# Performance work log

Measured on AMD Instinct MI355X. Metric: run time of the kernel, lower is better.

The kernel has to match this reference:

```python
import jax, jax.numpy as jnp
import numpy as np

N_P, N_I, DIM = 30, 40, 6
W_I, C1, C2, LAM = 0.7, 1.5, 1.5, 0.3
EPS = 1e-8


def _decode(pos):
    # pos: [P, 6] -> per-particle fusion weights via pairwise softmax
    e = jnp.exp(pos[:, :4])
    fg_s = e[:, 0] + e[:, 1] + EPS
    bg_s = e[:, 2] + e[:, 3] + EPS
    return e[:, 0] / fg_s, e[:, 1] / fg_s, e[:, 2] / bg_s, e[:, 3] / bg_s


def _fitness(pos, rgb, dep, mask, r_dep):
    # rgb, dep, mask, r_dep: [H, W]; pos: [P, 6] -> scores [P]
    rgb_fg, dep_fg, rgb_bg, dep_bg = _decode(pos)
    mn = mask - mask.mean()
    mn_norm = jnp.linalg.norm(mn) + EPS
    fg = rgb_fg[:, None, None] * rgb + dep_fg[:, None, None] * dep   # [P,H,W]
    bg = rgb_bg[:, None, None] * rgb + dep_bg[:, None, None] * dep
    fused = mask * fg + (1.0 - mask) * bg
    fn = fused - fused.mean(axis=(1, 2), keepdims=True)
    fn_norm = jnp.sqrt((fn * fn).sum(axis=(1, 2)))
    ncc = (fn * mn).sum(axis=(1, 2)) / (fn_norm * mn_norm + EPS)
    pen_fg = ((1.0 - r_dep) * mask).mean()
    pen_bg = ((1.0 - r_dep) * (1.0 - mask)).mean()
    rel_pen = dep_fg * pen_fg + dep_bg * pen_bg
    return ncc - LAM * rel_pen


def _pso(rgb, dep, mask, r_dep):
    # Deterministic PSO with fixed RNG key; inputs are [H, W] maps.
    key = jax.random.key(42)
    k_pos, k_vel, k_r1, k_r2 = jax.random.split(key, 4)
    pos = jax.random.uniform(k_pos, (N_P, DIM), minval=-2.0, maxval=2.0)
    vel = jax.random.uniform(k_vel, (N_P, DIM), minval=-0.5, maxval=0.5)
    r1s = jax.random.uniform(k_r1, (N_I, N_P, DIM))
    r2s = jax.random.uniform(k_r2, (N_I, N_P, DIM))

    pb_pos = pos
    pb_fit = _fitness(pos, rgb, dep, mask, r_dep)
    gi = jnp.argmax(pb_fit)
    gb_pos = pb_pos[gi]
    gb_fit = pb_fit[gi]

    def step(carry, rs):
        pos, vel, pb_pos, pb_fit, gb_pos, gb_fit = carry
        r1, r2 = rs
        vel = W_I * vel + C1 * r1 * (pb_pos - pos) + C2 * r2 * (gb_pos - pos)
        pos = jnp.clip(pos + vel, -3.0, 3.0)
        fit = _fitness(pos, rgb, dep, mask, r_dep)
        better = fit > pb_fit
        pb_pos = jnp.where(better[:, None], pos, pb_pos)
        pb_fit = jnp.where(better, fit, pb_fit)
        bi = jnp.argmax(pb_fit)
        improve = pb_fit[bi] > gb_fit
        gb_pos = jnp.where(improve, pb_pos[bi], gb_pos)
        gb_fit = jnp.where(improve, pb_fit[bi], gb_fit)
        return (pos, vel, pb_pos, pb_fit, gb_pos, gb_fit), None

    (pos, vel, pb_pos, pb_fit, gb_pos, gb_fit), _ = jax.lax.scan(
        step, (pos, vel, pb_pos, pb_fit, gb_pos, gb_fit), (r1s, r2s))
    rgb_fg, dep_fg, rgb_bg, dep_bg = _decode(gb_pos[None, :])
    return rgb_fg[0], dep_fg[0], rgb_bg[0], dep_bg[0]


def _cos_sim(feat, proto):
    # feat [B,C,H,W], proto [B,C] -> [B,H,W]; matches F.normalize (clamp_min eps)
    p = proto / jnp.maximum(jnp.linalg.norm(proto, axis=1, keepdims=True), 1e-12)
    fnorm = jnp.maximum(jnp.sqrt((feat * feat).sum(axis=1, keepdims=True)), 1e-12)
    f = feat / fnorm
    return jnp.einsum('bchw,bc->bhw', f, p)


def setup_inputs() -> dict:
    key = jax.random.key(0)
    ks = jax.random.split(key, 10)
    B, C, H, W = 8, 256, 64, 64
    return {
        'f_rgb': jax.random.normal(ks[0], (B, C, H, W), dtype=jnp.float32),
        'f_depth': jax.random.normal(ks[1], (B, C, H, W), dtype=jnp.float32),
        'r_rgb': jax.random.uniform(ks[2], (B, 1, H, W), dtype=jnp.float32),
        'r_depth': jax.random.uniform(ks[3], (B, 1, H, W), dtype=jnp.float32),
        'proto_rgb': jax.random.normal(ks[4], (B, C), dtype=jnp.float32),
        'proto_dep': jax.random.normal(ks[5], (B, C), dtype=jnp.float32),
        'query_mask': jax.random.uniform(ks[6], (B, 1, H, W), dtype=jnp.float32),
        'conv_w': jax.random.normal(ks[7], (C, C), dtype=jnp.float32) * 0.05,
        'bn_gamma': jax.random.uniform(ks[8], (C,), dtype=jnp.float32),
        'bn_beta': jax.random.normal(ks[9], (C,), dtype=jnp.float32) * 0.1,
        'bn_mean': jnp.zeros((C,), dtype=jnp.float32),
        'bn_var': jnp.ones((C,), dtype=jnp.float32),
    }


def reference(f_rgb, f_depth, r_rgb, r_depth, proto_rgb, proto_dep, query_mask,
              conv_w, bn_gamma, bn_beta, bn_mean, bn_var):
    # cosine similarity maps [B,H,W]
    rgb_sim = _cos_sim(f_rgb, proto_rgb)
    dep_sim = _cos_sim(f_depth, proto_dep)

    # PSO operates on detached batch-mean maps (torch .detach().mean(0).cpu())
    sg = jax.lax.stop_gradient
    np_rgb = sg(rgb_sim).mean(axis=0)                 # [H,W]
    np_dep = sg(dep_sim).mean(axis=0)                 # [H,W]
    np_mask = sg(query_mask)[:, 0].mean(axis=0)       # mask already at (H,W): nearest interp is identity
    np_r_dep = sg(r_depth)[:, 0].mean(axis=0)
    rgb_fg, dep_fg, rgb_bg, dep_bg = _pso(np_rgb, np_dep, np_mask, np_r_dep)

    f_fg = rgb_fg * f_rgb + dep_fg * f_depth
    f_bg = rgb_bg * f_rgb + dep_bg * f_depth
    proxy = jax.nn.sigmoid((rgb_sim + dep_sim)[:, None] * 3.0)   # [B,1,H,W]
    f_fused = proxy * f_fg + (1.0 - proxy) * f_bg

    # post_proj: 1x1 conv (no bias) -> BN (eval) -> ReLU
    y = jnp.einsum('oc,bchw->bohw', conv_w, f_fused)
    inv = bn_gamma / jnp.sqrt(bn_var + 1e-5)
    y = y * inv[None, :, None, None] + (bn_beta - bn_mean * inv)[None, :, None, None]
    return jax.nn.relu(y)
```

## Files before the change

kernel.cpp:

```cpp
#include <hip/hip_runtime.h>
#include <stdint.h>
#include <float.h>

static constexpr size_t WS_SIM_RGB = 4096;
static constexpr size_t WS_SIM_DEP = 36864;
static constexpr size_t WS_NPMAPS  = 69632;
static constexpr size_t WS_SYNC    = 86048;
static constexpr size_t WS_RNG     = 90112;

typedef short short8 __attribute__((ext_vector_type(8)));
typedef float f32x4 __attribute__((ext_vector_type(4)));

static constexpr uint32_t SYNC_MAGIC = 0x5A17C0DEu;

__device__ __forceinline__ uint32_t pack_bf2(float a, float b) {
  uint32_t ua = __float_as_uint(a), ub = __float_as_uint(b);
  uint32_t ra = (ua + 0x7fffu + ((ua >> 16) & 1u)) >> 16;
  uint32_t rb = (ub + 0x7fffu + ((ub >> 16) & 1u)) >> 16;
  return (ra & 0xffffu) | (rb << 16);
}

__device__ __forceinline__ void threefry2x32(uint32_t k0, uint32_t k1,
                                             uint32_t c0, uint32_t c1,
                                             uint32_t& o0, uint32_t& o1) {
  uint32_t ks2 = k0 ^ k1 ^ 0x1BD11BDAu;
  uint32_t x0 = c0 + k0;
  uint32_t x1 = c1 + k1;
#define TF_ROUND(r) { x0 += x1; x1 = (x1 << (r)) | (x1 >> (32 - (r))); x1 ^= x0; }
  TF_ROUND(13) TF_ROUND(15) TF_ROUND(26) TF_ROUND(6)
  x0 += k1;  x1 += ks2 + 1u;
  TF_ROUND(17) TF_ROUND(29) TF_ROUND(16) TF_ROUND(24)
  x0 += ks2; x1 += k0 + 2u;
  TF_ROUND(13) TF_ROUND(15) TF_ROUND(26) TF_ROUND(6)
  x0 += k0;  x1 += k1 + 3u;
  TF_ROUND(17) TF_ROUND(29) TF_ROUND(16) TF_ROUND(24)
  x0 += k1;  x1 += ks2 + 4u;
  TF_ROUND(13) TF_ROUND(15) TF_ROUND(26) TF_ROUND(6)
  x0 += ks2; x1 += k0 + 5u;
#undef TF_ROUND
  o0 = x0; o1 = x1;
}

__device__ __forceinline__ float tf_u01(uint32_t k0, uint32_t k1, uint32_t idx) {
  uint32_t o0, o1;
  threefry2x32(k0, k1, 0u, idx, o0, o1);
  uint32_t bits = o0 ^ o1;
  uint32_t fb = (bits >> 9) | 0x3F800000u;
  return __uint_as_float(fb) - 1.0f;
}

__global__ __launch_bounds__(256) void sim_kernel(
    const float* __restrict__ f_rgb, const float* __restrict__ f_dep,
    const float* __restrict__ proto_rgb, const float* __restrict__ proto_dep,
    float* __restrict__ sim_rgb, float* __restrict__ sim_dep) {
  int tid = threadIdx.x;
  int bm = blockIdx.y;
  int b = bm >> 1, mo = bm & 1;
  const float* f  = mo ? f_dep : f_rgb;
  const float* pr = mo ? proto_dep : proto_rgb;
  float* sim = mo ? sim_dep : sim_rgb;
  __shared__ float shp[256];
  __shared__ float wsum[4];
  float pv = pr[b * 256 + tid];
  float ss0 = pv * pv;
#pragma unroll
  for (int off = 32; off > 0; off >>= 1) ss0 += __shfl_xor(ss0, off, 64);
  if ((tid & 63) == 0) wsum[tid >> 6] = ss0;
  __syncthreads();
  float nrm = fmaxf(sqrtf(wsum[0] + wsum[1] + wsum[2] + wsum[3]), 1e-12f);
  shp[tid] = pv / nrm;
  __syncthreads();
  int p = blockIdx.x * 256 + tid;
  const float* base = f + (size_t)b * 256 * 4096 + p;
  float dot = 0.f, ss = 0.f;
#pragma unroll 8
  for (int c = 0; c < 256; ++c) {
    float x = base[(size_t)c * 4096];
    dot += x * shp[c];
    ss  += x * x;
  }
  float fn = fmaxf(sqrtf(ss), 1e-12f);
  sim[b * 4096 + p] = dot / fn;
}

__global__ __launch_bounds__(256) void npmaps_kernel(
    const float* __restrict__ sim_rgb, const float* __restrict__ sim_dep,
    const float* __restrict__ qmask, const float* __restrict__ r_dep,
    float* __restrict__ npm) {
  int i = blockIdx.x * 256 + threadIdx.x;
  float sr = 0.f, sd = 0.f, sm = 0.f, sq = 0.f;
#pragma unroll
  for (int b = 0; b < 8; ++b) {
    sr += sim_rgb[b * 4096 + i];
    sd += sim_dep[b * 4096 + i];
    sm += qmask[b * 4096 + i];
    sq += r_dep[b * 4096 + i];
  }
  npm[i]          = sr * 0.125f;
  npm[4096 + i]   = sd * 0.125f;
  npm[8192 + i]   = sm * 0.125f;
  npm[12288 + i]  = sq * 0.125f;
}

__global__ __launch_bounds__(256) void rng_kernel(float* __restrict__ rng) {
  int g = blockIdx.x * 256 + threadIdx.x;
  if (g >= 14760) return;
  int kind; uint32_t splitIdx, ctr, dst;
  if (g < 180) {
    kind = 0; splitIdx = 0; ctr = (uint32_t)g; dst = (uint32_t)g;
  } else if (g < 360) {
    kind = 1; splitIdx = 1; ctr = (uint32_t)(g - 180); dst = (uint32_t)g;
  } else if (g < 7560) {
    uint32_t c = (uint32_t)(g - 360);
    kind = 2; splitIdx = 2; ctr = c;
    uint32_t t = c / 180u, rem = c % 180u, p = rem / 6u, d = rem % 6u;
    dst = 360u + t * 360u + p * 12u + d;
  } else {
    uint32_t c = (uint32_t)(g - 7560);
    kind = 3; splitIdx = 3; ctr = c;
    uint32_t t = c / 180u, rem = c % 180u, p = rem / 6u, d = rem % 6u;
    dst = 360u + t * 360u + p * 12u + 6u + d;
  }
  uint32_t k0, k1;
  threefry2x32(0u, 42u, 0u, splitIdx, k0, k1);
  float u = tf_u01(k0, k1, ctr);
  float v;
  if (kind == 0)      v = fmaxf(-2.0f, u * 4.0f - 2.0f);
  else if (kind == 1) v = fmaxf(-0.5f, u - 0.5f);
  else                v = u;
  rng[dst] = v;
}

__device__ __forceinline__ float pso_fitness_fast(const float pos[6],
    const float S[4], const float G[16], const float V[4],
    float mn_norm, float pen_fg, float pen_bg) {
  float e0 = __expf(pos[0]), e1 = __expf(pos[1]);
  float e2 = __expf(pos[2]), e3 = __expf(pos[3]);
  float rf = __builtin_amdgcn_rcpf(e0 + e1 + 1e-8f);
  float rb = __builtin_amdgcn_rcpf(e2 + e3 + 1e-8f);
  float w[4] = {e0 * rf, e1 * rf, e2 * rb, e3 * rb};
  float num = 0.f, mus = 0.f;
#pragma unroll
  for (int k = 0; k < 4; ++k) { num += w[k] * V[k]; mus += w[k] * S[k]; }
  float q = 0.f;
#pragma unroll
  for (int j = 0; j < 4; ++j)
#pragma unroll
    for (int k = 0; k < 4; ++k) q += w[j] * G[j * 4 + k] * w[k];
  float fn2 = fmaxf(q - mus * mus * (1.f / 4096.f), 0.f);
  float den = __builtin_amdgcn_sqrtf(fn2) * mn_norm + 1e-8f;
  float ncc = num * __builtin_amdgcn_rcpf(den);
  return ncc - 0.3f * (w[1] * pen_fg + w[3] * pen_bg);
}

__device__ __forceinline__ float wavemax_lo32(float v) {
  int x = __float_as_int(v);
#define DPP_STEP(ctrl) { \
    int y = __builtin_amdgcn_update_dpp(x, x, ctrl, 0xf, 0xf, false); \
    x = __float_as_int(fmaxf(__int_as_float(x), __int_as_float(y))); }
  DPP_STEP(0x128)
  DPP_STEP(0x124)
  DPP_STEP(0x122)
  DPP_STEP(0x121)
#undef DPP_STEP
  float r0 = __int_as_float(__builtin_amdgcn_readlane(x, 0));
  float r1 = __int_as_float(__builtin_amdgcn_readlane(x, 16));
  return fmaxf(r0, r1);
}

__global__ __launch_bounds__(256, 4) void mega_kernel(
    const float* __restrict__ f_rgb, const float* __restrict__ f_dep,
    const float* __restrict__ sim_rgb, const float* __restrict__ sim_dep,
    const float* __restrict__ npm, const float* __restrict__ rng,
    const float* __restrict__ W,
    const float* __restrict__ bn_g, const float* __restrict__ bn_b,
    const float* __restrict__ bn_m, const float* __restrict__ bn_v,
    uint32_t* __restrict__ sync, float* __restrict__ out) {
  __shared__ __align__(16) uint32_t smem[4736];
  const int tid = threadIdx.x;
  const int bid = blockIdx.x;

  if (bid == 0) {
    float* colf = (float*)smem;
    float* res1 = colf + 17 * 257;
    float* res2 = res1 + 17;
    float* sst  = res2 + 5;
    const float* np_rgb  = npm;
    const float* np_dep  = npm + 4096;
    const float* np_mask = npm + 8192;
    const float* np_rdep = npm + 12288;
    {
      float acc[17];
#pragma unroll
      for (int k = 0; k < 17; ++k) acc[k] = 0.f;
      for (int i = tid; i < 4096; i += 256) {
        float m = np_mask[i], r = np_rgb[i], d = np_dep[i], q = np_rdep[i];
        float om = 1.f - m;
        float M1 = m * r, M2 = m * d, M3 = om * r, M4 = om * d;
        acc[0] += m;
        acc[1] += M1; acc[2] += M2; acc[3] += M3; acc[4] += M4;
        acc[5] += M1 * M1; acc[6] += M1 * M2; acc[7] += M1 * M3; acc[8] += M1 * M4;
        acc[9] += M2 * M2; acc[10] += M2 * M3; acc[11] += M2 * M4;
        acc[12] += M3 * M3; acc[13] += M3 * M4; acc[14] += M4 * M4;
        float oq = 1.f - q;
        acc[15] += oq * m; acc[16] += oq * om;
      }
#pragma unroll
      for (int k = 0; k < 17; ++k) colf[k * 257 + tid] = acc[k];
      __syncthreads();
      if (tid < 17) { float s = 0.f; for (int i = 0; i < 256; ++i) s += colf[tid * 257 + i]; res1[tid] = s; }
      __syncthreads();
      float mask_mean = res1[0] * (1.f / 4096.f);
      float a2[5] = {0.f, 0.f, 0.f, 0.f, 0.f};
      for (int i = tid; i < 4096; i += 256) {
        float m = np_mask[i], r = np_rgb[i], d = np_dep[i];
        float om = 1.f - m;
        float mn = m - mask_mean;
        a2[0] += m * r * mn; a2[1] += m * d * mn;
        a2[2] += om * r * mn; a2[3] += om * d * mn;
        a2[4] += mn * mn;
      }
      __syncthreads();
#pragma unroll
      for (int k = 0; k < 5; ++k) colf[k * 257 + tid] = a2[k];
      __syncthreads();
      if (tid < 5) { float s = 0.f; for (int i = 0; i < 256; ++i) s += colf[tid * 257 + i]; res2[tid] = s; }
      __syncthreads();
      if (tid == 0) {
        sst[0] = res1[1]; sst[1] = res1[2]; sst[2] = res1[3]; sst[3] = res1[4];
        float G11 = res1[5], G12 = res1[6], G13 = res1[7], G14 = res1[8];
        float G22 = res1[9], G23 = res1[10], G24 = res1[11];
        float G33 = res1[12], G34 = res1[13], G44 = res1[14];
        float Gf[16] = {G11, G12, G13, G14,  G12, G22, G23, G24,
                        G13, G23, G33, G34,  G14, G24, G34, G44};
        for (int k = 0; k < 16; ++k) sst[4 + k] = Gf[k];
        sst[20] = res2[0]; sst[21] = res2[1]; sst[22] = res2[2]; sst[23] = res2[3];
        sst[24] = sqrtf(res2[4]) + 1e-8f;
        sst[25] = res1[15] * (1.f / 4096.f);
        sst[26] = res1[16] * (1.f / 4096.f);
      }
      __syncthreads();
    }
    if (tid >= 64) return;
    int lane = tid;
    bool act = lane < 30;
    float S[4], G[16], V[4];
#pragma unroll
    for (int k = 0; k < 4; ++k) S[k] = sst[k];
#pragma unroll
    for (int k = 0; k < 16; ++k) G[k] = sst[4 + k];
#pragma unroll
    for (int k = 0; k < 4; ++k) V[k] = sst[20 + k];
    float mn_norm = sst[24], pen_fg = sst[25], pen_bg = sst[26];

    float pos[6], vel[6], pbp[6];
#pragma unroll
    for (int d = 0; d < 6; ++d) { pos[d] = 0.f; vel[d] = 0.f; }
    if (act) {
#pragma unroll
      for (int d = 0; d < 6; ++d) {
        pos[d] = rng[lane * 6 + d];
        vel[d] = rng[180 + lane * 6 + d];
      }
    }
#pragma unroll
    for (int d = 0; d < 6; ++d) pbp[d] = pos[d];

    float f0 = pso_fitness_fast(pos, S, G, V, mn_norm, pen_fg, pen_bg);
    float pbf = act ? f0 : -FLT_MAX;

    float gbf = wavemax_lo32(pbf);
    float gb[6];
    {
      unsigned long long mm = __ballot(pbf == gbf);
      int bl = __ffsll(mm) - 1;
#pragma unroll
      for (int d = 0; d < 6; ++d)
        gb[d] = __int_as_float(__builtin_amdgcn_readlane(__float_as_int(pbp[d]), bl));
    }

    const float* rbase = rng + 360;
    float4 A0, A1, A2, B0, B1, B2;
    {
      const float4* p0 = (const float4*)(rbase + lane * 12);
      A0 = p0[0]; A1 = p0[1]; A2 = p0[2];
      const float4* p1 = (const float4*)(rbase + 360 + lane * 12);
      B0 = p1[0]; B1 = p1[1]; B2 = p1[2];
    }

#define PSO_ITER(R0, R1, R2, TNEXT) { \
    float r1v[6] = {R0.x, R0.y, R0.z, R0.w, R1.x, R1.y}; \
    float r2v[6] = {R1.z, R1.w, R2.x, R2.y, R2.z, R2.w}; \
    const float4* pf = (const float4*)(rbase + (TNEXT) * 360 + lane * 12); \
    R0 = pf[0]; R1 = pf[1]; R2 = pf[2]; \
    _Pragma("unroll") \
    for (int d = 0; d < 6; ++d) { \
      vel[d] = 0.7f * vel[d] + 1.5f * r1v[d] * (pbp[d] - pos[d]) \
                             + 1.5f * r2v[d] * (gb[d] - pos[d]); \
      pos[d] = fmaxf(-3.0f, fminf(pos[d] + vel[d], 3.0f)); \
    } \
    float f = pso_fitness_fast(pos, S, G, V, mn_norm, pen_fg, pen_bg); \
    if (act && f > pbf) { \
      pbf = f; \
      _Pragma("unroll") for (int d = 0; d < 6; ++d) pbp[d] = pos[d]; \
    } \
    float maxv = wavemax_lo32(pbf); \
    if (maxv > gbf) {     \
      unsigned long long mm = __ballot(pbf == maxv); \
      int bl = __ffsll(mm) - 1; \
      gbf = maxv; \
      _Pragma("unroll") for (int d = 0; d < 6; ++d) \
        gb[d] = __int_as_float(__builtin_amdgcn_readlane(__float_as_int(pbp[d]), bl)); \
    } \
  }

    for (int k = 0; k < 20; ++k) {
      PSO_ITER(A0, A1, A2, 2 * k + 2)
      PSO_ITER(B0, B1, B2, 2 * k + 3)
    }
#undef PSO_ITER

    if (lane == 0) {
      float e0 = expf(gb[0]), e1 = expf(gb[1]), e2 = expf(gb[2]), e3 = expf(gb[3]);
      float fgs = e0 + e1 + 1e-8f, bgs = e2 + e3 + 1e-8f;
      uint32_t u0 = __float_as_uint(e0 / fgs);
      uint32_t u1 = __float_as_uint(e1 / fgs);
      uint32_t u2 = __float_as_uint(e2 / bgs);
      uint32_t u3 = __float_as_uint(e3 / bgs);
      atomicExch(&sync[0], u0);
      atomicExch(&sync[1], u1);
      atomicExch(&sync[2], u2);
      atomicExch(&sync[3], u3);
      __threadfence();
      atomicExch(&sync[4], u0 ^ u1 ^ u2 ^ u3 ^ SYNC_MAGIC);
    }
    return;
  }

  uint32_t* As = smem;
  uint32_t* BR = smem + 2560;
  uint32_t* BD = smem + 3648;
  const int gi = bid - 1;
  const int t0 = gi;
  const int t1 = (gi == 0) ? 1023 : -1;

  const int n4 = (tid & 15) * 4, kp = tid >> 4;
  const int am = tid & 127, kh = tid >> 7;
  const int lane = tid & 63, wv = tid >> 6;
  const int wm = wv >> 1, wn = wv & 1;
  const int lg = lane >> 4, ln = lane & 15;

  float pa = 0.f, pb_ = 0.f, pc_ = 0.f, pd_ = 0.f;
  bool have = false;

  for (int pass = 0; pass < 2; ++pass) {
    const int t = pass ? t1 : t0;
    if (t < 0) break;
    const int b = t >> 7, rem = t & 127, mt = rem >> 6, nt = rem & 63;
    const int m0 = mt * 128, n0 = nt * 64;
    const size_t fb = (size_t)b << 20;
    const float* frb = f_rgb + fb + n0 + n4;
    const float* fdb = f_dep + fb + n0 + n4;
    const float* wrow = W + (size_t)(m0 + am) * 256 + kh * 16;

    f32x4 accR[4][2], accD[4][2];
#pragma unroll
    for (int i = 0; i < 4; ++i)
#pragma unroll
      for (int j = 0; j < 2; ++j) { accR[i][j] = (f32x4)0.f; accD[i][j] = (f32x4)0.f; }

    for (int s8 = 0; s8 < 8; ++s8) {
      const int k0 = s8 * 32;
      {
        const size_t ko = (size_t)(k0 + 2 * kp) * 4096;
        const f32x4 r0 = *(const f32x4*)(frb + ko);
        const f32x4 r1 = *(const f32x4*)(frb + ko + 4096);
        const f32x4 d0 = *(const f32x4*)(fdb + ko);
        const f32x4 d1 = *(const f32x4*)(fdb + ko + 4096);
#pragma unroll
        for (int i2 = 0; i2 < 4; ++i2) {
          BR[(n4 + i2) * 17 + kp] = pack_bf2(r0[i2], r1[i2]);
          BD[(n4 + i2) * 17 + kp] = pack_bf2(d0[i2], d1[i2]);
        }
        const f32x4 w0 = *(const f32x4*)(wrow + k0);
        const f32x4 w1 = *(const f32x4*)(wrow + k0 + 4);
        const f32x4 w2 = *(const f32x4*)(wrow + k0 + 8);
        const f32x4 w3 = *(const f32x4*)(wrow + k0 + 12);
        uint32_t* ap = &As[am * 20 + kh * 8];
        ap[0] = pack_bf2(w0[0], w0[1]); ap[1] = pack_bf2(w0[2], w0[3]);
        ap[2] = pack_bf2(w1[0], w1[1]); ap[3] = pack_bf2(w1[2], w1[3]);
        ap[4] = pack_bf2(w2[0], w2[1]); ap[5] = pack_bf2(w2[2], w2[3]);
        ap[6] = pack_bf2(w3[0], w3[1]); ap[7] = pack_bf2(w3[2], w3[3]);
      }
      __syncthreads();
      short8 af[4], bfr[2], bfd[2];
#pragma unroll
      for (int i = 0; i < 4; ++i) {
        int m = wm * 64 + i * 16 + ln;
        float4 tq = *(const float4*)(&As[m * 20 + lg * 4]);
        af[i] = *(short8*)&tq;
      }
#pragma unroll
      for (int j = 0; j < 2; ++j) {
        int n = wn * 32 + j * 16 + ln;
        const uint32_t* bp = &BR[n * 17 + lg * 4];
        union { uint32_t w[4]; short8 v; } u;
        u.w[0] = bp[0]; u.w[1] = bp[1]; u.w[2] = bp[2]; u.w[3] = bp[3];
        bfr[j] = u.v;
        const uint32_t* dp = &BD[n * 17 + lg * 4];
        union { uint32_t w[4]; short8 v; } ud;
        ud.w[0] = dp[0]; ud.w[1] = dp[1]; ud.w[2] = dp[2]; ud.w[3] = dp[3];
        bfd[j] = ud.v;
      }
#pragma unroll
      for (int i = 0; i < 4; ++i)
#pragma unroll
        for (int j = 0; j < 2; ++j) {
          accR[i][j] = __builtin_amdgcn_mfma_f32_16x16x32_bf16(af[i], bfr[j], accR[i][j], 0, 0, 0);
          accD[i][j] = __builtin_amdgcn_mfma_f32_16x16x32_bf16(af[i], bfd[j], accD[i][j], 0, 0, 0);
        }
      __syncthreads();
    }

    if (!have) {
      if (tid == 0) {
        uint32_t a, b2, c, d, k;
        for (;;) {
          k  = atomicAdd(&sync[4], 0u);
          a  = atomicAdd(&sync[0], 0u);
          b2 = atomicAdd(&sync[1], 0u);
          c  = atomicAdd(&sync[2], 0u);
          d  = atomicAdd(&sync[3], 0u);
          if (k == (a ^ b2 ^ c ^ d ^ SYNC_MAGIC)) break;
          __builtin_amdgcn_s_sleep(32);
        }
        smem[0] = a; smem[1] = b2; smem[2] = c; smem[3] = d;
      }
      __syncthreads();
      pa  = __uint_as_float(smem[0]);
      pb_ = __uint_as_float(smem[1]);
      pc_ = __uint_as_float(smem[2]);
      pd_ = __uint_as_float(smem[3]);
      have = true;
      __syncthreads();
    }

    float abx0, aby0, abx1, aby1;
    {
      int nj0 = n0 + wn * 32 + ln;
      int nj1 = nj0 + 16;
      float s0 = sim_rgb[b * 4096 + nj0] + sim_dep[b * 4096 + nj0];
      float s1 = sim_rgb[b * 4096 + nj1] + sim_dep[b * 4096 + nj1];
      float pr0 = 1.f / (1.f + expf(-3.f * s0));
      float pr1 = 1.f / (1.f + expf(-3.f * s1));
      abx0 = pr0 * pa + (1.f - pr0) * pc_;  aby0 = pr0 * pb_ + (1.f - pr0) * pd_;
      abx1 = pr1 * pa + (1.f - pr1) * pc_;  aby1 = pr1 * pb_ + (1.f - pr1) * pd_;
    }
#pragma unroll
    for (int i = 0; i < 4; ++i) {
#pragma unroll
      for (int r = 0; r < 4; ++r) {
        int m = m0 + wm * 64 + i * 16 + lg * 4 + r;
        float inv = bn_g[m] / sqrtf(bn_v[m] + 1e-5f);
        float sh = bn_b[m] - bn_m[m] * inv;
        float* orow = out + ((size_t)(b * 256 + m)) * 4096 + n0 + wn * 32 + ln;
        float v0 = abx0 * accR[i][0][r] + aby0 * accD[i][0][r];
        float v1 = abx1 * accR[i][1][r] + aby1 * accD[i][1][r];
        orow[0]  = fmaxf(v0 * inv + sh, 0.f);
        orow[16] = fmaxf(v1 * inv + sh, 0.f);
      }
    }
    if (pass == 0 && t1 >= 0) __syncthreads();
  }
}

extern "C" void kernel_launch(void* const* d_in, const int* in_sizes, int n_in,
                              void* d_out, int out_size, void* d_ws, size_t ws_size,
                              hipStream_t stream) {
  (void)in_sizes; (void)n_in; (void)out_size; (void)ws_size;
  const float* f_rgb     = (const float*)d_in[0];
  const float* f_depth   = (const float*)d_in[1];
  const float* r_depth   = (const float*)d_in[3];
  const float* proto_rgb = (const float*)d_in[4];
  const float* proto_dep = (const float*)d_in[5];
  const float* qmask     = (const float*)d_in[6];
  const float* conv_w    = (const float*)d_in[7];
  const float* bn_g      = (const float*)d_in[8];
  const float* bn_b      = (const float*)d_in[9];
  const float* bn_m      = (const float*)d_in[10];
  const float* bn_v      = (const float*)d_in[11];
  float* out = (float*)d_out;
  float* ws  = (float*)d_ws;

  float* sim_rgb = ws + WS_SIM_RGB;
  float* sim_dep = ws + WS_SIM_DEP;
  float* npm     = ws + WS_NPMAPS;
  uint32_t* sync = (uint32_t*)(ws + WS_SYNC);
  float* rng     = ws + WS_RNG;

  rng_kernel<<<dim3(58), dim3(256), 0, stream>>>(rng);
  sim_kernel<<<dim3(16, 16), dim3(256), 0, stream>>>(f_rgb, f_depth, proto_rgb,
                                                     proto_dep, sim_rgb, sim_dep);
  npmaps_kernel<<<dim3(16), dim3(256), 0, stream>>>(sim_rgb, sim_dep, qmask, r_depth, npm);
  mega_kernel<<<dim3(1024), dim3(256), 0, stream>>>(f_rgb, f_depth, sim_rgb, sim_dep,
                                                    npm, rng, conv_w,
                                                    bn_g, bn_b, bn_m, bn_v, sync, out);
}
```

Measured before the change: 68.47 us.

## Fuse similarity, batch-mean maps and RNG generation into the persistent mega kernel

Removes the separate rng, similarity and batch-mean kernels and folds them into the single mega kernel. Block 0 now generates the RNG values itself, waits on per-chunk flags, and computes the batch means inline. The GEMM blocks with mt==0 compute the cosine similarities from the feature tiles they already load and publish each chunk with a magic flag. This cuts three launches and a second read of the features, but block 0 now serially depends on the flag spin-wait, and the flags are never reset between calls.

```diff
diff --git a/kernel.cpp b/kernel.cpp
--- a/kernel.cpp
+++ b/kernel.cpp
@@ -4,14 +4,15 @@
 
 static constexpr size_t WS_SIM_RGB = 4096;
 static constexpr size_t WS_SIM_DEP = 36864;
-static constexpr size_t WS_NPMAPS  = 69632;
 static constexpr size_t WS_SYNC    = 86048;
+static constexpr size_t WS_FLAGS   = 86560;
 static constexpr size_t WS_RNG     = 90112;
 
 typedef short short8 __attribute__((ext_vector_type(8)));
 typedef float f32x4 __attribute__((ext_vector_type(4)));
 
-static constexpr uint32_t SYNC_MAGIC = 0x5A17C0DEu;
+static constexpr uint32_t SYNC_MAGIC  = 0x5A17C0DEu;
+static constexpr uint32_t CHUNK_MAGIC = 0x600DF00Du;
 
 __device__ __forceinline__ uint32_t pack_bf2(float a, float b) {
   uint32_t ua = __float_as_uint(a), ub = __float_as_uint(b);
@@ -49,88 +50,6 @@
   return __uint_as_float(fb) - 1.0f;
 }
 
-__global__ __launch_bounds__(256) void sim_kernel(
-    const float* __restrict__ f_rgb, const float* __restrict__ f_dep,
-    const float* __restrict__ proto_rgb, const float* __restrict__ proto_dep,
-    float* __restrict__ sim_rgb, float* __restrict__ sim_dep) {
-  int tid = threadIdx.x;
-  int bm = blockIdx.y;
-  int b = bm >> 1, mo = bm & 1;
-  const float* f  = mo ? f_dep : f_rgb;
-  const float* pr = mo ? proto_dep : proto_rgb;
-  float* sim = mo ? sim_dep : sim_rgb;
-  __shared__ float shp[256];
-  __shared__ float wsum[4];
-  float pv = pr[b * 256 + tid];
-  float ss0 = pv * pv;
-#pragma unroll
-  for (int off = 32; off > 0; off >>= 1) ss0 += __shfl_xor(ss0, off, 64);
-  if ((tid & 63) == 0) wsum[tid >> 6] = ss0;
-  __syncthreads();
-  float nrm = fmaxf(sqrtf(wsum[0] + wsum[1] + wsum[2] + wsum[3]), 1e-12f);
-  shp[tid] = pv / nrm;
-  __syncthreads();
-  int p = blockIdx.x * 256 + tid;
-  const float* base = f + (size_t)b * 256 * 4096 + p;
-  float dot = 0.f, ss = 0.f;
-#pragma unroll 8
-  for (int c = 0; c < 256; ++c) {
-    float x = base[(size_t)c * 4096];
-    dot += x * shp[c];
-    ss  += x * x;
-  }
-  float fn = fmaxf(sqrtf(ss), 1e-12f);
-  sim[b * 4096 + p] = dot / fn;
-}
-
-__global__ __launch_bounds__(256) void npmaps_kernel(
-    const float* __restrict__ sim_rgb, const float* __restrict__ sim_dep,
-    const float* __restrict__ qmask, const float* __restrict__ r_dep,
-    float* __restrict__ npm) {
-  int i = blockIdx.x * 256 + threadIdx.x;
-  float sr = 0.f, sd = 0.f, sm = 0.f, sq = 0.f;
-#pragma unroll
-  for (int b = 0; b < 8; ++b) {
-    sr += sim_rgb[b * 4096 + i];
-    sd += sim_dep[b * 4096 + i];
-    sm += qmask[b * 4096 + i];
-    sq += r_dep[b * 4096 + i];
-  }
-  npm[i]          = sr * 0.125f;
-  npm[4096 + i]   = sd * 0.125f;
-  npm[8192 + i]   = sm * 0.125f;
-  npm[12288 + i]  = sq * 0.125f;
-}
-
-__global__ __launch_bounds__(256) void rng_kernel(float* __restrict__ rng) {
-  int g = blockIdx.x * 256 + threadIdx.x;
-  if (g >= 14760) return;
-  int kind; uint32_t splitIdx, ctr, dst;
-  if (g < 180) {
-    kind = 0; splitIdx = 0; ctr = (uint32_t)g; dst = (uint32_t)g;
-  } else if (g < 360) {
-    kind = 1; splitIdx = 1; ctr = (uint32_t)(g - 180); dst = (uint32_t)g;
-  } else if (g < 7560) {
-    uint32_t c = (uint32_t)(g - 360);
-    kind = 2; splitIdx = 2; ctr = c;
-    uint32_t t = c / 180u, rem = c % 180u, p = rem / 6u, d = rem % 6u;
-    dst = 360u + t * 360u + p * 12u + d;
-  } else {
-    uint32_t c = (uint32_t)(g - 7560);
-    kind = 3; splitIdx = 3; ctr = c;
-    uint32_t t = c / 180u, rem = c % 180u, p = rem / 6u, d = rem % 6u;
-    dst = 360u + t * 360u + p * 12u + 6u + d;
-  }
-  uint32_t k0, k1;
-  threefry2x32(0u, 42u, 0u, splitIdx, k0, k1);
-  float u = tf_u01(k0, k1, ctr);
-  float v;
-  if (kind == 0)      v = fmaxf(-2.0f, u * 4.0f - 2.0f);
-  else if (kind == 1) v = fmaxf(-0.5f, u - 0.5f);
-  else                v = u;
-  rng[dst] = v;
-}
-
 __device__ __forceinline__ float pso_fitness_fast(const float pos[6],
     const float S[4], const float G[16], const float V[4],
     float mn_norm, float pen_fg, float pen_bg) {
@@ -170,77 +89,123 @@
 
 __global__ __launch_bounds__(256, 4) void mega_kernel(
     const float* __restrict__ f_rgb, const float* __restrict__ f_dep,
-    const float* __restrict__ sim_rgb, const float* __restrict__ sim_dep,
-    const float* __restrict__ npm, const float* __restrict__ rng,
+    const float* __restrict__ qmask, const float* __restrict__ r_dep,
+    const float* __restrict__ proto_rgb, const float* __restrict__ proto_dep,
     const float* __restrict__ W,
     const float* __restrict__ bn_g, const float* __restrict__ bn_b,
     const float* __restrict__ bn_m, const float* __restrict__ bn_v,
-    uint32_t* __restrict__ sync, float* __restrict__ out) {
-  __shared__ __align__(16) uint32_t smem[4736];
+    float* __restrict__ sim_rgb, float* __restrict__ sim_dep,
+    float* __restrict__ rng, uint32_t* __restrict__ sync,
+    uint32_t* __restrict__ flags, float* __restrict__ out) {
+  __shared__ __align__(16) uint32_t smem[5264];
   const int tid = threadIdx.x;
   const int bid = blockIdx.x;
 
   if (bid == 0) {
-    float* colf = (float*)smem;
+    for (int j = 0; j < 58; ++j) {
+      int g = tid + 256 * j;
+      if (g < 14760) {
+        int kind; uint32_t splitIdx, ctr, dst;
+        if (g < 180)      { kind = 0; splitIdx = 0; ctr = (uint32_t)g; dst = (uint32_t)g; }
+        else if (g < 360) { kind = 1; splitIdx = 1; ctr = (uint32_t)(g - 180); dst = (uint32_t)g; }
+        else if (g < 7560) {
+          uint32_t c = (uint32_t)(g - 360);
+          kind = 2; splitIdx = 2; ctr = c;
+          uint32_t t = c / 180u, rem = c % 180u, p = rem / 6u, d = rem % 6u;
+          dst = 360u + t * 360u + p * 12u + d;
+        } else {
+          uint32_t c = (uint32_t)(g - 7560);
+          kind = 3; splitIdx = 3; ctr = c;
+          uint32_t t = c / 180u, rem = c % 180u, p = rem / 6u, d = rem % 6u;
+          dst = 360u + t * 360u + p * 12u + 6u + d;
+        }
+        uint32_t k0, k1;
+        threefry2x32(0u, 42u, 0u, splitIdx, k0, k1);
+        float u = tf_u01(k0, k1, ctr);
+        float v;
+        if (kind == 0)      v = fmaxf(-2.0f, u * 4.0f - 2.0f);
+        else if (kind == 1) v = fmaxf(-0.5f, u - 0.5f);
+        else                v = u;
+        rng[dst] = v;
+      }
+    }
+    for (;;) {
+      int ok = 1;
+      for (int k = tid; k < 512; k += 256)
+        ok &= (atomicAdd(&flags[k], 0u) == CHUNK_MAGIC) ? 1 : 0;
+      if (__syncthreads_count(ok) == 256) break;
+      __builtin_amdgcn_s_sleep(16);
+    }
+    __threadfence();
+    float* colf = (float*)(smem + 16);
     float* res1 = colf + 17 * 257;
     float* res2 = res1 + 17;
     float* sst  = res2 + 5;
-    const float* np_rgb  = npm;
-    const float* np_dep  = npm + 4096;
-    const float* np_mask = npm + 8192;
-    const float* np_rdep = npm + 12288;
-    {
-      float acc[17];
-#pragma unroll
-      for (int k = 0; k < 17; ++k) acc[k] = 0.f;
-      for (int i = tid; i < 4096; i += 256) {
-        float m = np_mask[i], r = np_rgb[i], d = np_dep[i], q = np_rdep[i];
-        float om = 1.f - m;
-        float M1 = m * r, M2 = m * d, M3 = om * r, M4 = om * d;
-        acc[0] += m;
-        acc[1] += M1; acc[2] += M2; acc[3] += M3; acc[4] += M4;
-        acc[5] += M1 * M1; acc[6] += M1 * M2; acc[7] += M1 * M3; acc[8] += M1 * M4;
-        acc[9] += M2 * M2; acc[10] += M2 * M3; acc[11] += M2 * M4;
-        acc[12] += M3 * M3; acc[13] += M3 * M4; acc[14] += M4 * M4;
-        float oq = 1.f - q;
-        acc[15] += oq * m; acc[16] += oq * om;
-      }
-#pragma unroll
-      for (int k = 0; k < 17; ++k) colf[k * 257 + tid] = acc[k];
-      __syncthreads();
-      if (tid < 17) { float s = 0.f; for (int i = 0; i < 256; ++i) s += colf[tid * 257 + i]; res1[tid] = s; }
-      __syncthreads();
-      float mask_mean = res1[0] * (1.f / 4096.f);
-      float a2[5] = {0.f, 0.f, 0.f, 0.f, 0.f};
-      for (int i = tid; i < 4096; i += 256) {
-        float m = np_mask[i], r = np_rgb[i], d = np_dep[i];
-        float om = 1.f - m;
-        float mn = m - mask_mean;
-        a2[0] += m * r * mn; a2[1] += m * d * mn;
-        a2[2] += om * r * mn; a2[3] += om * d * mn;
-        a2[4] += mn * mn;
-      }
-      __syncthreads();
-#pragma unroll
-      for (int k = 0; k < 5; ++k) colf[k * 257 + tid] = a2[k];
-      __syncthreads();
-      if (tid < 5) { float s = 0.f; for (int i = 0; i < 256; ++i) s += colf[tid * 257 + i]; res2[tid] = s; }
-      __syncthreads();
-      if (tid == 0) {
-        sst[0] = res1[1]; sst[1] = res1[2]; sst[2] = res1[3]; sst[3] = res1[4];
-        float G11 = res1[5], G12 = res1[6], G13 = res1[7], G14 = res1[8];
-        float G22 = res1[9], G23 = res1[10], G24 = res1[11];
-        float G33 = res1[12], G34 = res1[13], G44 = res1[14];
-        float Gf[16] = {G11, G12, G13, G14,  G12, G22, G23, G24,
-                        G13, G23, G33, G34,  G14, G24, G34, G44};
-        for (int k = 0; k < 16; ++k) sst[4 + k] = Gf[k];
-        sst[20] = res2[0]; sst[21] = res2[1]; sst[22] = res2[2]; sst[23] = res2[3];
-        sst[24] = sqrtf(res2[4]) + 1e-8f;
-        sst[25] = res1[15] * (1.f / 4096.f);
-        sst[26] = res1[16] * (1.f / 4096.f);
-      }
-      __syncthreads();
-    }
+    float acc[17];
+#pragma unroll
+    for (int k = 0; k < 17; ++k) acc[k] = 0.f;
+    for (int i = tid; i < 4096; i += 256) {
+      float sr = 0.f, sd = 0.f, sm = 0.f, sq = 0.f;
+#pragma unroll
+      for (int b = 0; b < 8; ++b) {
+        sr += sim_rgb[b * 4096 + i];
+        sd += sim_dep[b * 4096 + i];
+        sm += qmask[b * 4096 + i];
+        sq += r_dep[b * 4096 + i];
+      }
+      float r = sr * 0.125f, d = sd * 0.125f, m = sm * 0.125f, q = sq * 0.125f;
+      float om = 1.f - m;
+      float M1 = m * r, M2 = m * d, M3 = om * r, M4 = om * d;
+      acc[0] += m;
+      acc[1] += M1; acc[2] += M2; acc[3] += M3; acc[4] += M4;
+      acc[5] += M1 * M1; acc[6] += M1 * M2; acc[7] += M1 * M3; acc[8] += M1 * M4;
+      acc[9] += M2 * M2; acc[10] += M2 * M3; acc[11] += M2 * M4;
+      acc[12] += M3 * M3; acc[13] += M3 * M4; acc[14] += M4 * M4;
+      float oq = 1.f - q;
+      acc[15] += oq * m; acc[16] += oq * om;
+    }
+#pragma unroll
+    for (int k = 0; k < 17; ++k) colf[k * 257 + tid] = acc[k];
+    __syncthreads();
+    if (tid < 17) { float s = 0.f; for (int i = 0; i < 256; ++i) s += colf[tid * 257 + i]; res1[tid] = s; }
+    __syncthreads();
+    float mask_mean = res1[0] * (1.f / 4096.f);
+    float a2[5] = {0.f, 0.f, 0.f, 0.f, 0.f};
+    for (int i = tid; i < 4096; i += 256) {
+      float sr = 0.f, sd = 0.f, sm = 0.f;
+#pragma unroll
+      for (int b = 0; b < 8; ++b) {
+        sr += sim_rgb[b * 4096 + i];
+        sd += sim_dep[b * 4096 + i];
+        sm += qmask[b * 4096 + i];
+      }
+      float r = sr * 0.125f, d = sd * 0.125f, m = sm * 0.125f;
+      float om = 1.f - m;
+      float mn = m - mask_mean;
+      a2[0] += m * r * mn; a2[1] += m * d * mn;
+      a2[2] += om * r * mn; a2[3] += om * d * mn;
+      a2[4] += mn * mn;
+    }
+    __syncthreads();
+#pragma unroll
+    for (int k = 0; k < 5; ++k) colf[k * 257 + tid] = a2[k];
+    __syncthreads();
+    if (tid < 5) { float s = 0.f; for (int i = 0; i < 256; ++i) s += colf[tid * 257 + i]; res2[tid] = s; }
+    __syncthreads();
+    if (tid == 0) {
+      sst[0] = res1[1]; sst[1] = res1[2]; sst[2] = res1[3]; sst[3] = res1[4];
+      float G11 = res1[5], G12 = res1[6], G13 = res1[7], G14 = res1[8];
+      float G22 = res1[9], G23 = res1[10], G24 = res1[11];
+      float G33 = res1[12], G34 = res1[13], G44 = res1[14];
+      float Gf[16] = {G11, G12, G13, G14,  G12, G22, G23, G24,
+                      G13, G23, G33, G34,  G14, G24, G34, G44};
+      for (int k = 0; k < 16; ++k) sst[4 + k] = Gf[k];
+      sst[20] = res2[0]; sst[21] = res2[1]; sst[22] = res2[2]; sst[23] = res2[3];
+      sst[24] = sqrtf(res2[4]) + 1e-8f;
+      sst[25] = res1[15] * (1.f / 4096.f);
+      sst[26] = res1[16] * (1.f / 4096.f);
+    }
+    __syncthreads();
     if (tid >= 64) return;
     int lane = tid;
     bool act = lane < 30;
@@ -305,7 +270,7 @@
       _Pragma("unroll") for (int d = 0; d < 6; ++d) pbp[d] = pos[d]; \
     } \
     float maxv = wavemax_lo32(pbf); \
-    if (maxv > gbf) {     \
+    if (maxv > gbf) { \
       unsigned long long mm = __ballot(pbf == maxv); \
       int bl = __ffsll(mm) - 1; \
       gbf = maxv; \
@@ -337,12 +302,14 @@
     return;
   }
 
-  uint32_t* As = smem;
-  uint32_t* BR = smem + 2560;
-  uint32_t* BD = smem + 3648;
-  const int gi = bid - 1;
-  const int t0 = gi;
-  const int t1 = (gi == 0) ? 1023 : -1;
+  uint32_t* As = smem + 528;
+  uint32_t* BR = smem + 3088;
+  uint32_t* BD = smem + 4176;
+  float* PN      = (float*)(smem + 4);
+  float* protoRn = (float*)(smem + 16);
+  float* protoDn = (float*)(smem + 272);
+  const int gi0 = bid - 1;
+  const int t1v = (gi0 == 0) ? 1023 : -1;
 
   const int n4 = (tid & 15) * 4, kp = tid >> 4;
   const int am = tid & 127, kh = tid >> 7;
@@ -354,7 +321,7 @@
   bool have = false;
 
   for (int pass = 0; pass < 2; ++pass) {
-    const int t = pass ? t1 : t0;
+    const int t = pass ? t1v : gi0;
     if (t < 0) break;
     const int b = t >> 7, rem = t & 127, mt = rem >> 6, nt = rem & 63;
     const int m0 = mt * 128, n0 = nt * 64;
@@ -362,12 +329,33 @@
     const float* frb = f_rgb + fb + n0 + n4;
     const float* fdb = f_dep + fb + n0 + n4;
     const float* wrow = W + (size_t)(m0 + am) * 256 + kh * 16;
+    const bool do_sim = (mt == 0);
+
+    if (do_sim) {
+      float pvR = proto_rgb[b * 256 + tid];
+      float pvD = proto_dep[b * 256 + tid];
+      float sR = pvR * pvR, sD = pvD * pvD;
+#pragma unroll
+      for (int off = 32; off > 0; off >>= 1) {
+        sR += __shfl_xor(sR, off, 64);
+        sD += __shfl_xor(sD, off, 64);
+      }
+      if ((tid & 63) == 0) { PN[tid >> 6] = sR; PN[4 + (tid >> 6)] = sD; }
+      __syncthreads();
+      float nR = fmaxf(sqrtf(PN[0] + PN[1] + PN[2] + PN[3]), 1e-12f);
+      float nD = fmaxf(sqrtf(PN[4] + PN[5] + PN[6] + PN[7]), 1e-12f);
+      protoRn[tid] = pvR / nR;
+      protoDn[tid] = pvD / nD;
+      __syncthreads();
+    }
 
     f32x4 accR[4][2], accD[4][2];
 #pragma unroll
     for (int i = 0; i < 4; ++i)
 #pragma unroll
       for (int j = 0; j < 2; ++j) { accR[i][j] = (f32x4)0.f; accD[i][j] = (f32x4)0.f; }
+    float dotR[4] = {0.f, 0.f, 0.f, 0.f}, ssR[4] = {0.f, 0.f, 0.f, 0.f};
+    float dotD[4] = {0.f, 0.f, 0.f, 0.f}, ssD[4] = {0.f, 0.f, 0.f, 0.f};
 
     for (int s8 = 0; s8 < 8; ++s8) {
       const int k0 = s8 * 32;
@@ -377,6 +365,18 @@
         const f32x4 r1 = *(const f32x4*)(frb + ko + 4096);
         const f32x4 d0 = *(const f32x4*)(fdb + ko);
         const f32x4 d1 = *(const f32x4*)(fdb + ko + 4096);
+        if (do_sim) {
+          const int c0 = k0 + 2 * kp;
+          float pR0 = protoRn[c0], pR1 = protoRn[c0 + 1];
+          float pD0 = protoDn[c0], pD1 = protoDn[c0 + 1];
+#pragma unroll
+          for (int i2 = 0; i2 < 4; ++i2) {
+            dotR[i2] += r0[i2] * pR0 + r1[i2] * pR1;
+            ssR[i2]  += r0[i2] * r0[i2] + r1[i2] * r1[i2];
+            dotD[i2] += d0[i2] * pD0 + d1[i2] * pD1;
+            ssD[i2]  += d0[i2] * d0[i2] + d1[i2] * d1[i2];
+          }
+        }
 #pragma unroll
         for (int i2 = 0; i2 < 4; ++i2) {
           BR[(n4 + i2) * 17 + kp] = pack_bf2(r0[i2], r1[i2]);
@@ -422,6 +422,33 @@
       __syncthreads();
     }
 
+    if (do_sim) {
+      float* part = (float*)(smem + 528);
+#pragma unroll
+      for (int i2 = 0; i2 < 4; ++i2) {
+        part[tid * 17 + i2]      = dotR[i2];
+        part[tid * 17 + 4 + i2]  = ssR[i2];
+        part[tid * 17 + 8 + i2]  = dotD[i2];
+        part[tid * 17 + 12 + i2] = ssD[i2];
+      }
+      __syncthreads();
+      if (tid < 128) {
+        int mo = tid & 1, p = tid >> 1;
+        int g = p >> 2, i2 = p & 3;
+        float dot = 0.f, ss = 0.f;
+#pragma unroll
+        for (int kk = 0; kk < 16; ++kk) {
+          const float* pp = &part[(g + 16 * kk) * 17 + mo * 8];
+          dot += pp[i2];
+          ss  += pp[4 + i2];
+        }
+        float fn = fmaxf(sqrtf(ss), 1e-12f);
+        (mo ? sim_dep : sim_rgb)[b * 4096 + n0 + p] = dot / fn;
+      }
+      __syncthreads();
+      if (tid == 0) { __threadfence(); atomicExch(&flags[b * 64 + nt], CHUNK_MAGIC); }
+    }
+
     if (!have) {
       if (tid == 0) {
         uint32_t a, b2, c, d, k;
@@ -434,6 +461,7 @@
           if (k == (a ^ b2 ^ c ^ d ^ SYNC_MAGIC)) break;
           __builtin_amdgcn_s_sleep(32);
         }
+        __threadfence();
         smem[0] = a; smem[1] = b2; smem[2] = c; smem[3] = d;
       }
       __syncthreads();
@@ -470,7 +498,7 @@
         orow[16] = fmaxf(v1 * inv + sh, 0.f);
       }
     }
-    if (pass == 0 && t1 >= 0) __syncthreads();
+    if (pass == 0 && t1v >= 0) __syncthreads();
   }
 }
 
@@ -492,17 +520,13 @@
   float* out = (float*)d_out;
   float* ws  = (float*)d_ws;
 
-  float* sim_rgb = ws + WS_SIM_RGB;
-  float* sim_dep = ws + WS_SIM_DEP;
-  float* npm     = ws + WS_NPMAPS;
-  uint32_t* sync = (uint32_t*)(ws + WS_SYNC);
-  float* rng     = ws + WS_RNG;
-
-  rng_kernel<<<dim3(58), dim3(256), 0, stream>>>(rng);
-  sim_kernel<<<dim3(16, 16), dim3(256), 0, stream>>>(f_rgb, f_depth, proto_rgb,
-                                                     proto_dep, sim_rgb, sim_dep);
-  npmaps_kernel<<<dim3(16), dim3(256), 0, stream>>>(sim_rgb, sim_dep, qmask, r_depth, npm);
-  mega_kernel<<<dim3(1024), dim3(256), 0, stream>>>(f_rgb, f_depth, sim_rgb, sim_dep,
-                                                    npm, rng, conv_w,
-                                                    bn_g, bn_b, bn_m, bn_v, sync, out);
-}
+  float* sim_rgb  = ws + WS_SIM_RGB;
+  float* sim_dep  = ws + WS_SIM_DEP;
+  uint32_t* sync  = (uint32_t*)(ws + WS_SYNC);
+  uint32_t* flags = (uint32_t*)(ws + WS_FLAGS);
+  float* rng      = ws + WS_RNG;
+
+  mega_kernel<<<dim3(1024), dim3(256), 0, stream>>>(
+      f_rgb, f_depth, qmask, r_depth, proto_rgb, proto_dep, conv_w,
+      bn_g, bn_b, bn_m, bn_v, sim_rgb, sim_dep, rng, sync, flags, out);
+}
```

After: 126.4 us. +84.6%, slower.

## Double-buffer GEMM shared-memory tiles with register prefetch of next K-step

Applied to the files above, without the earlier changes.

The K loop of the fused GEMM now prefetches the next step's global loads into registers before running the current step's MFMAs. It packs them into an alternate shared-memory buffer afterwards, which removes one __syncthreads per iteration. The goal is to overlap global-memory latency with the matrix math. Shared memory roughly doubles (about 37 KB), which may lower occupancy under launch_bounds(256,4), and more registers stay live. The tiles move past a 16-word header so the sync scalars no longer alias the tiles, and a threadfence is added after the spin-wait.

```diff
diff --git a/kernel.cpp b/kernel.cpp
--- a/kernel.cpp
+++ b/kernel.cpp
@@ -176,12 +176,12 @@
     const float* __restrict__ bn_g, const float* __restrict__ bn_b,
     const float* __restrict__ bn_m, const float* __restrict__ bn_v,
     uint32_t* __restrict__ sync, float* __restrict__ out) {
-  __shared__ __align__(16) uint32_t smem[4736];
+  __shared__ __align__(16) uint32_t smem[9488];
   const int tid = threadIdx.x;
   const int bid = blockIdx.x;
 
   if (bid == 0) {
-    float* colf = (float*)smem;
+    float* colf = (float*)(smem + 16);
     float* res1 = colf + 17 * 257;
     float* res2 = res1 + 17;
     float* sst  = res2 + 5;
@@ -337,9 +337,9 @@
     return;
   }
 
-  uint32_t* As = smem;
-  uint32_t* BR = smem + 2560;
-  uint32_t* BD = smem + 3648;
+  uint32_t* As = smem + 16;
+  uint32_t* BR = smem + 5136;
+  uint32_t* BD = smem + 7312;
   const int gi = bid - 1;
   const int t0 = gi;
   const int t1 = (gi == 0) ? 1023 : -1;
@@ -369,45 +369,57 @@
 #pragma unroll
       for (int j = 0; j < 2; ++j) { accR[i][j] = (f32x4)0.f; accD[i][j] = (f32x4)0.f; }
 
+    f32x4 vr0, vr1, vd0, vd1, vw0, vw1, vw2, vw3;
+
+#define LOAD_STEP(S) { \
+    const size_t ko = (size_t)((S) * 32 + 2 * kp) * 4096; \
+    vr0 = *(const f32x4*)(frb + ko); \
+    vr1 = *(const f32x4*)(frb + ko + 4096); \
+    vd0 = *(const f32x4*)(fdb + ko); \
+    vd1 = *(const f32x4*)(fdb + ko + 4096); \
+    vw0 = *(const f32x4*)(wrow + (S) * 32); \
+    vw1 = *(const f32x4*)(wrow + (S) * 32 + 4); \
+    vw2 = *(const f32x4*)(wrow + (S) * 32 + 8); \
+    vw3 = *(const f32x4*)(wrow + (S) * 32 + 12); \
+  }
+
+#define PACK_WRITE(BUF) { \
+    uint32_t* brp = &BR[(BUF) * 1088]; \
+    uint32_t* bdp = &BD[(BUF) * 1088]; \
+    _Pragma("unroll") \
+    for (int i2 = 0; i2 < 4; ++i2) { \
+      brp[(n4 + i2) * 17 + kp] = pack_bf2(vr0[i2], vr1[i2]); \
+      bdp[(n4 + i2) * 17 + kp] = pack_bf2(vd0[i2], vd1[i2]); \
+    } \
+    uint32_t* ap = &As[(BUF) * 2560 + am * 20 + kh * 8]; \
+    ap[0] = pack_bf2(vw0[0], vw0[1]); ap[1] = pack_bf2(vw0[2], vw0[3]); \
+    ap[2] = pack_bf2(vw1[0], vw1[1]); ap[3] = pack_bf2(vw1[2], vw1[3]); \
+    ap[4] = pack_bf2(vw2[0], vw2[1]); ap[5] = pack_bf2(vw2[2], vw2[3]); \
+    ap[6] = pack_bf2(vw3[0], vw3[1]); ap[7] = pack_bf2(vw3[2], vw3[3]); \
+  }
+
+    LOAD_STEP(0)
+    PACK_WRITE(0)
+    __syncthreads();
+
     for (int s8 = 0; s8 < 8; ++s8) {
-      const int k0 = s8 * 32;
-      {
-        const size_t ko = (size_t)(k0 + 2 * kp) * 4096;
-        const f32x4 r0 = *(const f32x4*)(frb + ko);
-        const f32x4 r1 = *(const f32x4*)(frb + ko + 4096);
-        const f32x4 d0 = *(const f32x4*)(fdb + ko);
-        const f32x4 d1 = *(const f32x4*)(fdb + ko + 4096);
-#pragma unroll
-        for (int i2 = 0; i2 < 4; ++i2) {
-          BR[(n4 + i2) * 17 + kp] = pack_bf2(r0[i2], r1[i2]);
-          BD[(n4 + i2) * 17 + kp] = pack_bf2(d0[i2], d1[i2]);
-        }
-        const f32x4 w0 = *(const f32x4*)(wrow + k0);
-        const f32x4 w1 = *(const f32x4*)(wrow + k0 + 4);
-        const f32x4 w2 = *(const f32x4*)(wrow + k0 + 8);
-        const f32x4 w3 = *(const f32x4*)(wrow + k0 + 12);
-        uint32_t* ap = &As[am * 20 + kh * 8];
-        ap[0] = pack_bf2(w0[0], w0[1]); ap[1] = pack_bf2(w0[2], w0[3]);
-        ap[2] = pack_bf2(w1[0], w1[1]); ap[3] = pack_bf2(w1[2], w1[3]);
-        ap[4] = pack_bf2(w2[0], w2[1]); ap[5] = pack_bf2(w2[2], w2[3]);
-        ap[6] = pack_bf2(w3[0], w3[1]); ap[7] = pack_bf2(w3[2], w3[3]);
-      }
-      __syncthreads();
+      const int cur = s8 & 1;
+      if (s8 < 7) LOAD_STEP(s8 + 1)
       short8 af[4], bfr[2], bfd[2];
 #pragma unroll
       for (int i = 0; i < 4; ++i) {
         int m = wm * 64 + i * 16 + ln;
-        float4 tq = *(const float4*)(&As[m * 20 + lg * 4]);
+        float4 tq = *(const float4*)(&As[cur * 2560 + m * 20 + lg * 4]);
         af[i] = *(short8*)&tq;
       }
 #pragma unroll
       for (int j = 0; j < 2; ++j) {
         int n = wn * 32 + j * 16 + ln;
-        const uint32_t* bp = &BR[n * 17 + lg * 4];
+        const uint32_t* bp = &BR[cur * 1088 + n * 17 + lg * 4];
         union { uint32_t w[4]; short8 v; } u;
         u.w[0] = bp[0]; u.w[1] = bp[1]; u.w[2] = bp[2]; u.w[3] = bp[3];
         bfr[j] = u.v;
-        const uint32_t* dp = &BD[n * 17 + lg * 4];
+        const uint32_t* dp = &BD[cur * 1088 + n * 17 + lg * 4];
         union { uint32_t w[4]; short8 v; } ud;
         ud.w[0] = dp[0]; ud.w[1] = dp[1]; ud.w[2] = dp[2]; ud.w[3] = dp[3];
         bfd[j] = ud.v;
@@ -419,8 +431,11 @@
           accR[i][j] = __builtin_amdgcn_mfma_f32_16x16x32_bf16(af[i], bfr[j], accR[i][j], 0, 0, 0);
           accD[i][j] = __builtin_amdgcn_mfma_f32_16x16x32_bf16(af[i], bfd[j], accD[i][j], 0, 0, 0);
         }
-      __syncthreads();
-    }
+      if (s8 < 7) PACK_WRITE(cur ^ 1)
+      __syncthreads();
+    }
+#undef LOAD_STEP
+#undef PACK_WRITE
 
     if (!have) {
       if (tid == 0) {
@@ -434,6 +449,7 @@
           if (k == (a ^ b2 ^ c ^ d ^ SYNC_MAGIC)) break;
           __builtin_amdgcn_s_sleep(32);
         }
+        __threadfence();
         smem[0] = a; smem[1] = b2; smem[2] = c; smem[3] = d;
       }
       __syncthreads();
```

After: 122.4 us. +78.7%, slower.
